# Performance work log

Measured on AMD Instinct MI355X. Metric: run time of the kernel, lower is better.

Reference implementation:

```python
import jax, jax.numpy as jnp
import numpy as np

N = 100000   # nodes
E = 3200000  # edges
IN = 5
H = 128
L = 6
EPS = 1e-5

def _bn(x, g, b):
    # BatchNorm1d in training mode: batch stats over node dim, biased variance
    m = jnp.mean(x, axis=0)
    v = jnp.mean((x - m) ** 2, axis=0)
    return (x - m) * jax.lax.rsqrt(v + EPS) * g + b

def setup_inputs() -> dict:
    key = jax.random.key(0)
    ks = jax.random.split(key, 20)
    x = jax.random.normal(ks[0], (N, IN), dtype=jnp.float32)
    edge_index = jax.random.randint(ks[1], (2, E), 0, N, dtype=jnp.int64)
    batch = jnp.zeros((N,), dtype=jnp.int64)
    s = 0.05
    return {
        "x": x, "edge_index": edge_index, "batch": batch,
        "in_W": jax.random.normal(ks[2], (IN, H), jnp.float32) * s,
        "in_b": jnp.zeros((H,), jnp.float32),
        "in_g": jnp.ones((H,), jnp.float32),
        "in_beta": jnp.zeros((H,), jnp.float32),
        "conv_W": jax.random.normal(ks[3], (L, H, H), jnp.float32) * s,
        "conv_b": jnp.zeros((L, H), jnp.float32),
        "bn_g": jnp.ones((L, H), jnp.float32),
        "bn_beta": jnp.zeros((L, H), jnp.float32),
        "pW1": jax.random.normal(ks[4], (H, 32), jnp.float32) * s,
        "pb1": jnp.zeros((32,), jnp.float32),
        "pW2": jax.random.normal(ks[5], (32, 1), jnp.float32) * s,
        "pb2": jnp.zeros((1,), jnp.float32),
        "vW1": jax.random.normal(ks[6], (H, 64), jnp.float32) * s,
        "vb1": jnp.zeros((64,), jnp.float32),
        "vW2": jax.random.normal(ks[7], (64, 1), jnp.float32) * s,
        "vb2": jnp.zeros((1,), jnp.float32),
    }

def reference(x, edge_index, batch, in_W, in_b, in_g, in_beta,
              conv_W, conv_b, bn_g, bn_beta,
              pW1, pb1, pW2, pb2, vW1, vb1, vW2, vb2):
    n = x.shape[0]
    # GCN normalization with self-loops (computed once; depends only on edge_index)
    loops = jnp.arange(n, dtype=edge_index.dtype)
    src = jnp.concatenate([edge_index[0], loops])
    dst = jnp.concatenate([edge_index[1], loops])
    deg = jax.ops.segment_sum(jnp.ones_like(dst, dtype=x.dtype), dst, num_segments=n)
    dinv = jnp.where(deg > 0, jax.lax.rsqrt(deg), 0.0)
    norm = dinv[src] * dinv[dst]  # [E+N]

    def gcn(h, W, b):
        h = h @ W
        msg = h[src] * norm[:, None]
        return jax.ops.segment_sum(msg, dst, num_segments=n) + b

    h = jax.nn.relu(_bn(x @ in_W + in_b, in_g, in_beta))
    for i in range(L):
        h = jax.nn.relu(_bn(gcn(h, conv_W[i], conv_b[i]), bn_g[i], bn_beta[i])) + h

    policy_logits = (jax.nn.relu(h @ pW1 + pb1) @ pW2 + pb2)[:, 0]  # [N]

    # global_mean_pool over batch ids (single graph here, num_segments=1)
    num_graphs = 1
    sums = jax.ops.segment_sum(h, batch, num_segments=num_graphs)
    cnts = jax.ops.segment_sum(jnp.ones((n,), h.dtype), batch, num_segments=num_graphs)
    g = sums / jnp.maximum(cnts, 1.0)[:, None]  # [1, H]
    value = jnp.tanh(jax.nn.relu(g @ vW1 + vb1) @ vW2 + vb2)[:, 0]  # [1]
    return policy_logits, value
```

## Files before the change

### kernel.cpp

```cpp
#include <hip/hip_runtime.h>
#include <hip/hip_bf16.h>

typedef __hip_bfloat16 bf16;
typedef long long i64;
typedef unsigned short u16;
typedef __attribute__((ext_vector_type(8))) short bf16x8;
typedef __attribute__((ext_vector_type(4))) float f32x4;

#define EPSV 1e-5f
#define WINLEN 2560
#define CHUNK 64

static __device__ __forceinline__ float ldf(const void* p, size_t i, int fb) {
  return fb ? __bfloat162float(((const bf16*)p)[i]) : ((const float*)p)[i];
}
static __device__ __forceinline__ u16 f2b(float f) {
  unsigned int u = __float_as_uint(f);
  u += 0x7FFF + ((u >> 16) & 1);
  return (u16)(u >> 16);
}
static __device__ __forceinline__ float rb2f(u16 u) {
  return __uint_as_float(((unsigned int)u) << 16);
}
static __device__ __forceinline__ unsigned pk2(float a, float b) {
  return (unsigned)f2b(a) | ((unsigned)f2b(b) << 16);
}
static __device__ __forceinline__ float lo2f(unsigned w) { return __uint_as_float(w << 16); }
static __device__ __forceinline__ float hi2f(unsigned w) { return __uint_as_float(w & 0xFFFF0000u); }


__global__ void setup_kernel(const int* __restrict__ ei_w, const unsigned int* __restrict__ g,
                             int* __restrict__ eflag, int* __restrict__ fflag,
                             int* __restrict__ degcnt, int* __restrict__ fill,
                             int* __restrict__ wctr, int n) {
  int i = blockIdx.x * 256 + threadIdx.x;
  if (i < n) { degcnt[i] = 0; fill[i] = 0; }
  if (blockIdx.x == 0) {
    __shared__ int nz;
    if (threadIdx.x == 0) nz = 0;
    if (threadIdx.x < 32) wctr[threadIdx.x] = 0;
    __syncthreads();
    for (int k = threadIdx.x; k < 1024; k += 256)
      if (ei_w[2 * k + 1] != 0) atomicAdd(&nz, 1);
    __syncthreads();
    if (threadIdx.x == 0) {
      *eflag = (nz == 0) ? 1 : 0;
      *fflag = (g[0] == 0x3F803F80u) ? 1 : 0;
    }
  }
}


__global__ void __launch_bounds__(256) pre_merged_kernel(
    const void* __restrict__ x, const void* __restrict__ W, const void* __restrict__ b,
    const void* __restrict__ ei, const void* __restrict__ convW,
    const int* __restrict__ eflag, const int* __restrict__ fflag,
    int* __restrict__ degcnt, u16* __restrict__ pre, float* __restrict__ pi,
    u16* __restrict__ wf, int n, int in_dim, int e, int wtotal, int gi, int gf) {
  __shared__ float4 SS[256], QQ[256];
  int fb = *fflag;
  if ((int)blockIdx.x < gi) {
    int q = threadIdx.x & 31, g8 = threadIdx.x >> 5;
    int c = q * 4;
    float b0 = ldf(b, c, fb), b1 = ldf(b, c + 1, fb), b2v = ldf(b, c + 2, fb), b3 = ldf(b, c + 3, fb);
    float s0 = 0, s1 = 0, s2 = 0, s3 = 0, q0 = 0, q1 = 0, q2 = 0, q3 = 0;
    for (int node = blockIdx.x * 8 + g8; node < n; node += gi * 8) {
      float a0 = b0, a1 = b1, a2 = b2v, a3 = b3;
      for (int k = 0; k < in_dim; ++k) {
        float xv = ldf(x, (size_t)node * in_dim + k, fb);
        size_t w0 = (size_t)k * 128 + c;
        a0 = fmaf(xv, ldf(W, w0, fb), a0);
        a1 = fmaf(xv, ldf(W, w0 + 1, fb), a1);
        a2 = fmaf(xv, ldf(W, w0 + 2, fb), a2);
        a3 = fmaf(xv, ldf(W, w0 + 3, fb), a3);
      }
      unsigned w0p = pk2(a0, a1), w1p = pk2(a2, a3);
      *(uint2*)(pre + (size_t)node * 128 + c) = make_uint2(w0p, w1p);
      float r0 = lo2f(w0p), r1 = hi2f(w0p), r2 = lo2f(w1p), r3 = hi2f(w1p);
      s0 += r0; s1 += r1; s2 += r2; s3 += r3;
      q0 = fmaf(r0, r0, q0); q1 = fmaf(r1, r1, q1); q2 = fmaf(r2, r2, q2); q3 = fmaf(r3, r3, q3);
    }
    SS[threadIdx.x] = make_float4(s0, s1, s2, s3);
    QQ[threadIdx.x] = make_float4(q0, q1, q2, q3);
    __syncthreads();
    if (threadIdx.x < 32) {
      float4 a = SS[threadIdx.x], qq = QQ[threadIdx.x];
      for (int g = 1; g < 8; ++g) {
        float4 u = SS[g * 32 + threadIdx.x], w = QQ[g * 32 + threadIdx.x];
        a.x += u.x; a.y += u.y; a.z += u.z; a.w += u.w;
        qq.x += w.x; qq.y += w.y; qq.z += w.z; qq.w += w.w;
      }
      int cc = threadIdx.x * 4;
      *(float4*)(pi + (size_t)blockIdx.x * 256 + cc) = a;
      *(float4*)(pi + (size_t)blockIdx.x * 256 + 128 + cc) = qq;
    }
  } else if ((int)blockIdx.x < gi + gf) {
    int bid = blockIdx.x - gi;
    int k = bid & 7;
    int lo = (int)(((long long)n * k) >> 3);
    int hi = (int)(((long long)n * (k + 1)) >> 3);
    int stride = (gf >> 3) * 256;
    int fb64 = *eflag;
    for (int i = (bid >> 3) * 256 + threadIdx.x; i < e; i += stride) {
      int d;
      if (fb64) d = (int)((const i64*)ei)[(size_t)e + i];
      else      d = ((const int*)ei)[(size_t)e + i];
      if (d >= lo && d < hi) atomicAdd(&degcnt[d], 1);
    }
  } else {
    int bid = blockIdx.x - gi - gf;
    int i = bid * 256 + threadIdx.x;
    if (i < wtotal) {
      int l = i >> 14, r = i & 16383;
      int k = r >> 7, nn = r & 127;
      int s = k >> 5, quad = (k >> 3) & 3, j = k & 7;
      int ct = nn >> 4, n16 = nn & 15;
      wf[(size_t)l * 16384 + (ct * 4 + s) * 512 + quad * 128 + n16 * 8 + j] = f2b(ldf(convW, i, fb));
    }
  }
}


__global__ void __launch_bounds__(256) scanA_kernel(const int* __restrict__ deg,
                                                    int* __restrict__ rp,
                                                    int* __restrict__ bsum,
                                                    float* __restrict__ dinv, int n) {
  int base = blockIdx.x * 1024 + threadIdx.x * 4;
  int v0 = (base     < n) ? deg[base]     : 0;
  int v1 = (base + 1 < n) ? deg[base + 1] : 0;
  int v2 = (base + 2 < n) ? deg[base + 2] : 0;
  int v3 = (base + 3 < n) ? deg[base + 3] : 0;
  if (base     < n) dinv[base]     = rsqrtf((float)v0 + 1.0f);
  if (base + 1 < n) dinv[base + 1] = rsqrtf((float)v1 + 1.0f);
  if (base + 2 < n) dinv[base + 2] = rsqrtf((float)v2 + 1.0f);
  if (base + 3 < n) dinv[base + 3] = rsqrtf((float)v3 + 1.0f);
  int ts = v0 + v1 + v2 + v3;
  __shared__ int ls[256];
  ls[threadIdx.x] = ts;
  __syncthreads();
  for (int off = 1; off < 256; off <<= 1) {
    int u = (threadIdx.x >= off) ? ls[threadIdx.x - off] : 0;
    __syncthreads();
    ls[threadIdx.x] += u;
    __syncthreads();
  }
  int run = ls[threadIdx.x] - ts;
  if (base     < n) rp[base]     = run; run += v0;
  if (base + 1 < n) rp[base + 1] = run; run += v1;
  if (base + 2 < n) rp[base + 2] = run; run += v2;
  if (base + 3 < n) rp[base + 3] = run;
  if (threadIdx.x == 255) bsum[blockIdx.x] = ls[255];
}

__global__ void __launch_bounds__(256) scanB_kernel(int* __restrict__ bsum, int* __restrict__ rp,
                                                    int nb, int n, int e) {
  __shared__ int ls[256];
  int t = threadIdx.x;
  int v = (t < nb) ? bsum[t] : 0;
  ls[t] = v;
  __syncthreads();
  for (int off = 1; off < 256; off <<= 1) {
    int u = (t >= off) ? ls[t - off] : 0;
    __syncthreads();
    ls[t] += u;
    __syncthreads();
  }
  if (t < nb) bsum[t] = ls[t] - v;
  if (t == 0) rp[n] = e;
}

__global__ void scanC_kernel(int* __restrict__ rp, const int* __restrict__ bsum, int n) {
  int i = blockIdx.x * 256 + threadIdx.x;
  if (i < n) rp[i] += bsum[i >> 10];
}

__global__ void fill_kernel(const void* __restrict__ ei, const int* __restrict__ flag,
                            const int* __restrict__ row_ptr,
                            int* __restrict__ fill, int* __restrict__ csr_src, int e, int n) {
  int k = blockIdx.x & 7;
  int lo = (int)(((long long)n * k) >> 3);
  int hi = (int)(((long long)n * (k + 1)) >> 3);
  int stride = (gridDim.x >> 3) * 256;
  int fb64 = *flag;
  for (int i = (blockIdx.x >> 3) * 256 + threadIdx.x; i < e; i += stride) {
    int d;
    if (fb64) d = (int)((const i64*)ei)[(size_t)e + i];
    else      d = ((const int*)ei)[(size_t)e + i];
    if (d < lo || d >= hi) continue;
    int s;
    if (fb64) s = (int)((const i64*)ei)[i];
    else      s = ((const int*)ei)[i];
    int pos = row_ptr[d] + atomicAdd(&fill[d], 1);
    csr_src[pos] = s;
  }
}

__global__ void __launch_bounds__(1024) finalize_inproj_kernel(
    const float* __restrict__ pi, int nb,
    const void* __restrict__ g, const void* __restrict__ beta,
    const int* __restrict__ fflag,
    float* __restrict__ scale, float* __restrict__ shift,
    float inv_n) {
  __shared__ float RS[8][128], RQ[8][128];
  int fb = *fflag;
  int c = threadIdx.x & 127, r = threadIdx.x >> 7;
  float s = 0.f, s2 = 0.f;
#pragma unroll 4
  for (int b = r; b < nb; b += 8) {
    s  += pi[(size_t)b * 256 + c];
    s2 += pi[(size_t)b * 256 + 128 + c];
  }
  RS[r][c] = s; RQ[r][c] = s2;
  __syncthreads();
  if (threadIdx.x < 128) {
    float ts = 0.f, tq = 0.f;
#pragma unroll
    for (int i = 0; i < 8; ++i) { ts += RS[i][c]; tq += RQ[i][c]; }
    float mean = ts * inv_n;
    float var = tq * inv_n - mean * mean;
    float sc = ldf(g, c, fb) * rsqrtf(var + EPSV);
    scale[c] = sc;
    shift[c] = ldf(beta, c, fb) - mean * sc;
  }
}


__global__ void __launch_bounds__(256) gemm_bn_kernel(
    const u16* __restrict__ pre, u16* __restrict__ hbuf,
    const float* __restrict__ scale, const float* __restrict__ shift,
    const u16* __restrict__ wfL, const float* __restrict__ dinv,
    u16* __restrict__ u, int n, int use_res) {
  __shared__ u16 At[4][2048];
  int lane = threadIdx.x & 63;
  int wave = threadIdx.x >> 6;
  int n16 = lane & 15, quad = lane >> 4;
  u16* at = At[wave];
  int node = lane & 15;
  int cgrp = lane >> 4;
  int ntiles = (n + 15) >> 4;
  for (int tile = blockIdx.x * 4 + wave; tile < ntiles; tile += gridDim.x * 4) {
    int n0 = tile * 16;
    int gn = n0 + node;
#pragma unroll
    for (int r = 0; r < 8; ++r) {
      int c4 = r * 4 + cgrp;
      int c = c4 * 4;
      float4 h4 = make_float4(0.f, 0.f, 0.f, 0.f);
      if (gn < n) {
        uint2 pv = *(const uint2*)(pre + (size_t)gn * 128 + c);
        float4 sc = *(const float4*)(scale + c);
        float4 sh = *(const float4*)(shift + c);
        h4.x = fmaxf(fmaf(lo2f(pv.x), sc.x, sh.x), 0.f);
        h4.y = fmaxf(fmaf(hi2f(pv.x), sc.y, sh.y), 0.f);
        h4.z = fmaxf(fmaf(lo2f(pv.y), sc.z, sh.z), 0.f);
        h4.w = fmaxf(fmaf(hi2f(pv.y), sc.w, sh.w), 0.f);
        if (use_res) {
          uint2 rv = *(const uint2*)(hbuf + (size_t)gn * 128 + c);
          h4.x += lo2f(rv.x); h4.y += hi2f(rv.x);
          h4.z += lo2f(rv.y); h4.w += hi2f(rv.y);
        }
        *(uint2*)(hbuf + (size_t)gn * 128 + c) = make_uint2(pk2(h4.x, h4.y), pk2(h4.z, h4.w));
      }
      ushort4 uu;
      uu.x = f2b(h4.x); uu.y = f2b(h4.y); uu.z = f2b(h4.z); uu.w = f2b(h4.w);
      int s = c4 >> 3, qd = (c4 >> 1) & 3, j0 = (c4 & 1) * 4;
      *(ushort4*)(at + s * 512 + qd * 128 + node * 8 + j0) = uu;
    }
    __builtin_amdgcn_s_waitcnt(0);
    f32x4 acc[8];
#pragma unroll
    for (int ct = 0; ct < 8; ++ct) acc[ct] = (f32x4){0.f, 0.f, 0.f, 0.f};
#pragma unroll
    for (int s = 0; s < 4; ++s) {
      bf16x8 af = *(const bf16x8*)(at + s * 512 + lane * 8);
#pragma unroll
      for (int ct = 0; ct < 8; ++ct) {
        bf16x8 bfr = *(const bf16x8*)(wfL + (size_t)(ct * 4 + s) * 512 + lane * 8);
        acc[ct] = __builtin_amdgcn_mfma_f32_16x16x32_bf16(af, bfr, acc[ct], 0, 0, 0);
      }
    }
    float dv[4];
#pragma unroll
    for (int r = 0; r < 4; ++r) {
      int row = n0 + quad * 4 + r;
      dv[r] = (row < n) ? dinv[row] : 0.f;
    }
#pragma unroll
    for (int ct = 0; ct < 8; ++ct) {
#pragma unroll
      for (int r = 0; r < 4; ++r) {
        int row = n0 + quad * 4 + r;
        if (row < n)
          u[((size_t)(ct >> 1) * n + row) * 32 + (ct & 1) * 16 + n16] = f2b(acc[ct][r] * dv[r]);
      }
    }
  }
}


__global__ void __launch_bounds__(256) gather_stats_kernel(
    const int* __restrict__ row_ptr, const int* __restrict__ csr_src,
    const u16* __restrict__ u, const float* __restrict__ dinv,
    const void* __restrict__ b, const int* __restrict__ fflag,
    u16* __restrict__ pre, float* __restrict__ pg,
    int* __restrict__ wctr, int n, int nch, size_t bOff) {
  __shared__ int sm[WINLEN];
  __shared__ float SW[4][4][8], QW[4][4][8];
  __shared__ int curchunk;
  int fb = *fflag;
  int ct2 = blockIdx.x & 3;
  const u16* us = u + (size_t)ct2 * n * 32;
  int q = threadIdx.x & 3;
  int g = threadIdx.x >> 2;
  int c = ct2 * 32 + q * 8;
  float bias[8];
#pragma unroll
  for (int i = 0; i < 8; ++i) bias[i] = ldf(b, bOff + c + i, fb);
  float sA[8], qA[8];
#pragma unroll
  for (int i = 0; i < 8; ++i) { sA[i] = 0.f; qA[i] = 0.f; }

  for (;;) {
    __syncthreads();
    if (threadIdx.x == 0) curchunk = atomicAdd(&wctr[ct2], 1);
    __syncthreads();
    int ch = curchunk;
    if (ch >= nch) break;
    int c0 = ch * CHUNK;
    int node = c0 + g;
    int valid = node < n;
    int beg = valid ? row_ptr[node] : 0;
    int end = valid ? row_ptr[node + 1] : 0;
    int cend = c0 + CHUNK; if (cend > n) cend = n;
    int chunk_lo = row_ptr[c0];
    int chunk_hi = row_ptr[cend];
    float acc[8];
    if (valid) {
      uint4 su = *(const uint4*)(us + (size_t)node * 32 + q * 8);
      acc[0] = lo2f(su.x); acc[1] = hi2f(su.x);
      acc[2] = lo2f(su.y); acc[3] = hi2f(su.y);
      acc[4] = lo2f(su.z); acc[5] = hi2f(su.z);
      acc[6] = lo2f(su.w); acc[7] = hi2f(su.w);
    } else {
#pragma unroll
      for (int i = 0; i < 8; ++i) acc[i] = 0.f;
    }
    for (int wlo = chunk_lo; wlo < chunk_hi; wlo += WINLEN) {
      int wlen = chunk_hi - wlo; if (wlen > WINLEN) wlen = WINLEN;
      __syncthreads();
      for (int i = threadIdx.x; i < wlen; i += 256)
        sm[i] = __builtin_nontemporal_load(csr_src + wlo + i);
      __syncthreads();
      int j0 = beg > wlo ? beg : wlo;
      int j1 = end < wlo + wlen ? end : wlo + wlen;
      int j = j0;
#define ACC(UU) \
      acc[0] += lo2f(UU.x); acc[1] += hi2f(UU.x); \
      acc[2] += lo2f(UU.y); acc[3] += hi2f(UU.y); \
      acc[4] += lo2f(UU.z); acc[5] += hi2f(UU.z); \
      acc[6] += lo2f(UU.w); acc[7] += hi2f(UU.w);
      for (; j + 8 <= j1; j += 8) {
        int i0 = sm[j - wlo],     i1 = sm[j - wlo + 1], i2 = sm[j - wlo + 2], i3 = sm[j - wlo + 3];
        int i4 = sm[j - wlo + 4], i5 = sm[j - wlo + 5], i6 = sm[j - wlo + 6], i7 = sm[j - wlo + 7];
        uint4 U0 = *(const uint4*)(us + (size_t)i0 * 32 + q * 8);
        uint4 U1 = *(const uint4*)(us + (size_t)i1 * 32 + q * 8);
        uint4 U2 = *(const uint4*)(us + (size_t)i2 * 32 + q * 8);
        uint4 U3 = *(const uint4*)(us + (size_t)i3 * 32 + q * 8);
        uint4 U4 = *(const uint4*)(us + (size_t)i4 * 32 + q * 8);
        uint4 U5 = *(const uint4*)(us + (size_t)i5 * 32 + q * 8);
        uint4 U6 = *(const uint4*)(us + (size_t)i6 * 32 + q * 8);
        uint4 U7 = *(const uint4*)(us + (size_t)i7 * 32 + q * 8);
        ACC(U0) ACC(U1) ACC(U2) ACC(U3) ACC(U4) ACC(U5) ACC(U6) ACC(U7)
      }
      for (; j + 4 <= j1; j += 4) {
        int i0 = sm[j - wlo], i1 = sm[j - wlo + 1], i2 = sm[j - wlo + 2], i3 = sm[j - wlo + 3];
        uint4 U0 = *(const uint4*)(us + (size_t)i0 * 32 + q * 8);
        uint4 U1 = *(const uint4*)(us + (size_t)i1 * 32 + q * 8);
        uint4 U2 = *(const uint4*)(us + (size_t)i2 * 32 + q * 8);
        uint4 U3 = *(const uint4*)(us + (size_t)i3 * 32 + q * 8);
        ACC(U0) ACC(U1) ACC(U2) ACC(U3)
      }
      for (; j < j1; ++j) {
        int i0 = sm[j - wlo];
        uint4 U0 = *(const uint4*)(us + (size_t)i0 * 32 + q * 8);
        ACC(U0)
      }
#undef ACC
    }
    if (valid) {
      float dv = dinv[node];
      float o0 = fmaf(acc[0], dv, bias[0]), o1 = fmaf(acc[1], dv, bias[1]);
      float o2 = fmaf(acc[2], dv, bias[2]), o3 = fmaf(acc[3], dv, bias[3]);
      float o4 = fmaf(acc[4], dv, bias[4]), o5 = fmaf(acc[5], dv, bias[5]);
      float o6 = fmaf(acc[6], dv, bias[6]), o7 = fmaf(acc[7], dv, bias[7]);
      unsigned w0 = pk2(o0, o1), w1 = pk2(o2, o3), w2 = pk2(o4, o5), w3 = pk2(o6, o7);
      *(uint4*)(pre + (size_t)node * 128 + c) = make_uint4(w0, w1, w2, w3);
      float r0 = lo2f(w0), r1 = hi2f(w0), r2 = lo2f(w1), r3 = hi2f(w1);
      float r4 = lo2f(w2), r5 = hi2f(w2), r6 = lo2f(w3), r7 = hi2f(w3);
      sA[0] += r0; sA[1] += r1; sA[2] += r2; sA[3] += r3;
      sA[4] += r4; sA[5] += r5; sA[6] += r6; sA[7] += r7;
      qA[0] = fmaf(r0, r0, qA[0]); qA[1] = fmaf(r1, r1, qA[1]);
      qA[2] = fmaf(r2, r2, qA[2]); qA[3] = fmaf(r3, r3, qA[3]);
      qA[4] = fmaf(r4, r4, qA[4]); qA[5] = fmaf(r5, r5, qA[5]);
      qA[6] = fmaf(r6, r6, qA[6]); qA[7] = fmaf(r7, r7, qA[7]);
    }
  }
#pragma unroll
  for (int m = 4; m <= 32; m <<= 1) {
#pragma unroll
    for (int i = 0; i < 8; ++i) {
      sA[i] += __shfl_xor(sA[i], m, 64);
      qA[i] += __shfl_xor(qA[i], m, 64);
    }
  }
  int lane = threadIdx.x & 63, wv = threadIdx.x >> 6;
  if (lane < 4) {
#pragma unroll
    for (int i = 0; i < 8; ++i) { SW[wv][lane][i] = sA[i]; QW[wv][lane][i] = qA[i]; }
  }
  __syncthreads();
  if (threadIdx.x < 32) {
    int qq = threadIdx.x >> 3, i = threadIdx.x & 7;
    float a = SW[0][qq][i] + SW[1][qq][i] + SW[2][qq][i] + SW[3][qq][i];
    float b2 = QW[0][qq][i] + QW[1][qq][i] + QW[2][qq][i] + QW[3][qq][i];
    pg[(size_t)blockIdx.x * 64 + qq * 8 + i] = a;
    pg[(size_t)blockIdx.x * 64 + 32 + qq * 8 + i] = b2;
  }
}

__global__ void __launch_bounds__(1024) finalize_gather_kernel(
    const float* __restrict__ pg, int nbG,
    const void* __restrict__ g, const void* __restrict__ beta,
    const int* __restrict__ fflag,
    float* __restrict__ scale, float* __restrict__ shift,
    float inv_n, size_t off) {
  __shared__ float RS[8][128], RQ[8][128];
  int fb = *fflag;
  int c = threadIdx.x & 127, r = threadIdx.x >> 7;
  int ct2 = c >> 5, ic = c & 31;
  float s = 0.f, s2 = 0.f;
#pragma unroll 4
  for (int b = ct2 + 4 * r; b < nbG; b += 32) {
    s  += pg[(size_t)b * 64 + ic];
    s2 += pg[(size_t)b * 64 + 32 + ic];
  }
  RS[r][c] = s; RQ[r][c] = s2;
  __syncthreads();
  if (threadIdx.x < 128) {
    float ts = 0.f, tq = 0.f;
#pragma unroll
    for (int i = 0; i < 8; ++i) { ts += RS[i][c]; tq += RQ[i][c]; }
    float mean = ts * inv_n;
    float var = tq * inv_n - mean * mean;
    float sc = ldf(g, off + c, fb) * rsqrtf(var + EPSV);
    scale[c] = sc;
    shift[c] = ldf(beta, off + c, fb) - mean * sc;
  }
}


__global__ void __launch_bounds__(256) policy_pool_kernel(
    const u16* __restrict__ pre, const u16* __restrict__ hbuf,
    const float* __restrict__ scale, const float* __restrict__ shift,
    const void* __restrict__ pW1, const void* __restrict__ pb1,
    const void* __restrict__ pW2, const void* __restrict__ pb2,
    const int* __restrict__ fflag, float* __restrict__ pp,
    void* __restrict__ out, int n) {
  __shared__ float W1[128 * 32];
  __shared__ float B1v[32], W2v[32];
  int fb = *fflag;
  for (int i = threadIdx.x; i < 128 * 32; i += 256) W1[i] = ldf(pW1, i, fb);
  if (threadIdx.x < 32) {
    B1v[threadIdx.x] = ldf(pb1, threadIdx.x, fb);
    W2v[threadIdx.x] = ldf(pW2, threadIdx.x, fb);
  }
  __syncthreads();
  float bias2 = ldf(pb2, 0, fb);
  int q = threadIdx.x & 31, g8 = threadIdx.x >> 5;
  int c = q * 4;
  float4 sc = *(const float4*)(scale + c);
  float4 sh = *(const float4*)(shift + c);
  float cs0 = 0, cs1 = 0, cs2 = 0, cs3 = 0;
  for (int node = blockIdx.x * 8 + g8; node < n; node += gridDim.x * 8) {
    uint2 pv = *(const uint2*)(pre + (size_t)node * 128 + c);
    uint2 rv = *(const uint2*)(hbuf + (size_t)node * 128 + c);
    float4 h4;
    h4.x = fmaxf(fmaf(lo2f(pv.x), sc.x, sh.x), 0.f) + lo2f(rv.x);
    h4.y = fmaxf(fmaf(hi2f(pv.x), sc.y, sh.y), 0.f) + hi2f(rv.x);
    h4.z = fmaxf(fmaf(lo2f(pv.y), sc.z, sh.z), 0.f) + lo2f(rv.y);
    h4.w = fmaxf(fmaf(hi2f(pv.y), sc.w, sh.w), 0.f) + hi2f(rv.y);
    cs0 += h4.x; cs1 += h4.y; cs2 += h4.z; cs3 += h4.w;
    float acc = B1v[q];
#pragma unroll
    for (int k4 = 0; k4 < 32; ++k4) {
      float hx = __shfl(h4.x, k4, 32);
      float hy = __shfl(h4.y, k4, 32);
      float hz = __shfl(h4.z, k4, 32);
      float hw = __shfl(h4.w, k4, 32);
      int k = k4 * 4;
      acc = fmaf(hx, W1[k * 32 + q], acc);
      acc = fmaf(hy, W1[(k + 1) * 32 + q], acc);
      acc = fmaf(hz, W1[(k + 2) * 32 + q], acc);
      acc = fmaf(hw, W1[(k + 3) * 32 + q], acc);
    }
    acc = fmaxf(acc, 0.f) * W2v[q];
    for (int off = 16; off; off >>= 1) acc += __shfl_down(acc, off, 32);
    if (q == 0) {
      float v = acc + bias2;
      if (fb) ((bf16*)out)[node] = __float2bfloat16(v);
      else    ((float*)out)[node] = v;
    }
  }
  __shared__ float4 SS[256];
  SS[threadIdx.x] = make_float4(cs0, cs1, cs2, cs3);
  __syncthreads();
  if (threadIdx.x < 32) {
    float4 a = SS[threadIdx.x];
    for (int g = 1; g < 8; ++g) {
      float4 u = SS[g * 32 + threadIdx.x];
      a.x += u.x; a.y += u.y; a.z += u.z; a.w += u.w;
    }
    *(float4*)(pp + (size_t)blockIdx.x * 128 + threadIdx.x * 4) = a;
  }
}

__global__ void __launch_bounds__(1024) value_kernel(
    const float* __restrict__ pp, int nbP,
    const void* __restrict__ vW1, const void* __restrict__ vb1,
    const void* __restrict__ vW2, const void* __restrict__ vb2,
    const int* __restrict__ fflag,
    void* __restrict__ out, int n, float inv_n) {
  __shared__ float RS[8][128];
  __shared__ float gs[128];
  int fb = *fflag;
  int c = threadIdx.x & 127, r = threadIdx.x >> 7;
  float s = 0.f;
#pragma unroll 4
  for (int b = r; b < nbP; b += 8) s += pp[(size_t)b * 128 + c];
  RS[r][c] = s;
  __syncthreads();
  if (threadIdx.x < 128) {
    float t = 0.f;
#pragma unroll
    for (int i = 0; i < 8; ++i) t += RS[i][c];
    gs[c] = t;
  }
  __syncthreads();
  if (threadIdx.x < 64) {
    int cc = threadIdx.x;
    float acc = ldf(vb1, cc, fb);
    for (int k = 0; k < 128; ++k) acc = fmaf(gs[k] * inv_n, ldf(vW1, (size_t)k * 64 + cc, fb), acc);
    acc = fmaxf(acc, 0.f);
    float v = acc * ldf(vW2, cc, fb);
    for (int off = 32; off; off >>= 1) v += __shfl_down(v, off, 64);
    if (cc == 0) {
      float rr = tanhf(v + ldf(vb2, 0, fb));
      if (fb) ((bf16*)out)[n] = __float2bfloat16(rr);
      else    ((float*)out)[n] = rr;
    }
  }
}


extern "C" void kernel_launch(void* const* d_in, const int* in_sizes, int n_in,
                              void* d_out, int out_size, void* d_ws, size_t ws_size,
                              hipStream_t stream) {
  const void* x       = d_in[0];
  const void* ei      = d_in[1];
  const void* in_W    = d_in[3];
  const void* in_b    = d_in[4];
  const void* in_g    = d_in[5];
  const void* in_beta = d_in[6];
  const void* conv_W  = d_in[7];
  const void* conv_b  = d_in[8];
  const void* bn_g    = d_in[9];
  const void* bn_beta = d_in[10];
  const void* pW1     = d_in[11];
  const void* pb1     = d_in[12];
  const void* pW2     = d_in[13];
  const void* pb2     = d_in[14];
  const void* vW1     = d_in[15];
  const void* vb1     = d_in[16];
  const void* vW2     = d_in[17];
  const void* vb2     = d_in[18];

  const int H = 128;
  int in_dim = in_sizes[3] / H;
  int n      = in_sizes[0] / in_dim;
  int e      = in_sizes[1] / 2;
  int L      = in_sizes[7] / (H * H);

  const int GS  = 2048;
  const int GI  = 512;
  const int GP  = 1024;
  const int GF  = 2048;

  char* w = (char*)d_ws;
  u16*   u    = (u16*)w;   w += (size_t)n * H * sizeof(u16);
  u16*   pre  = (u16*)w;   w += (size_t)n * H * sizeof(u16);
  u16*   hbuf = (u16*)w;   w += (size_t)n * H * sizeof(u16);
  int*   csr_src  = (int*)w;   w += ((size_t)e + 16) * sizeof(int);
  int*   row_ptr  = (int*)w;   w += (size_t)(n + 1 + 15) / 16 * 16 * sizeof(int);
  int*   degcnt   = (int*)w;   w += (size_t)n * sizeof(int);
  int*   fillc    = (int*)w;   w += (size_t)n * sizeof(int);
  float* dinv     = (float*)w; w += (size_t)n * sizeof(float);
  float* scale = (float*)w; w += 128 * sizeof(float);
  float* shift = (float*)w; w += 128 * sizeof(float);
  int*   eflag = (int*)w;   w += 16 * sizeof(int);
  int*   fflag = (int*)w;   w += 16 * sizeof(int);
  int*   bsum  = (int*)w;   w += 256 * sizeof(int);
  int*   wctr  = (int*)w;   w += 32 * sizeof(int);
  u16*   wf    = (u16*)w;   w += (size_t)L * H * H * sizeof(u16);
  float* pi    = (float*)w; w += (size_t)GI * 256 * sizeof(float);
  float* pg    = (float*)w; w += (size_t)GS * 64 * sizeof(float);
  float* pp    = (float*)w; w += (size_t)GP * 128 * sizeof(float);

  int gN = (n + 255) / 256;
  int nb = (n + 1023) >> 10;
  int nch = (n + CHUNK - 1) / CHUNK;
  int wtotal = L * H * H;
  int GW = (wtotal + 255) / 256;
  float inv_n = 1.0f / (float)n;

  setup_kernel<<<gN, 256, 0, stream>>>((const int*)ei, (const unsigned int*)in_g,
                                       eflag, fflag, degcnt, fillc, wctr, n);
  pre_merged_kernel<<<GI + GF + GW, 256, 0, stream>>>(
      x, in_W, in_b, ei, conv_W, eflag, fflag, degcnt, pre, pi, wf,
      n, in_dim, e, wtotal, GI, GF);
  scanA_kernel<<<nb, 256, 0, stream>>>(degcnt, row_ptr, bsum, dinv, n);
  scanB_kernel<<<1, 256, 0, stream>>>(bsum, row_ptr, nb, n, e);
  scanC_kernel<<<gN, 256, 0, stream>>>(row_ptr, bsum, n);
  fill_kernel<<<GF, 256, 0, stream>>>(ei, eflag, row_ptr, fillc, csr_src, e, n);
  finalize_inproj_kernel<<<1, 1024, 0, stream>>>(pi, GI, in_g, in_beta, fflag, scale, shift, inv_n);

  for (int l = 0; l < L; ++l) {
    gemm_bn_kernel<<<2048, 256, 0, stream>>>(pre, hbuf, scale, shift, wf + (size_t)l * H * H,
                                             dinv, u, n, (l > 0) ? 1 : 0);
    gather_stats_kernel<<<GS, 256, 0, stream>>>(row_ptr, csr_src, u, dinv,
                                                conv_b, fflag, pre, pg, wctr + l * 4,
                                                n, nch, (size_t)l * H);
    finalize_gather_kernel<<<1, 1024, 0, stream>>>(pg, GS, bn_g, bn_beta, fflag, scale, shift,
                                                   inv_n, (size_t)l * H);
  }

  policy_pool_kernel<<<GP, 256, 0, stream>>>(pre, hbuf, scale, shift, pW1, pb1, pW2, pb2,
                                             fflag, pp, d_out, n);
  value_kernel<<<1, 1024, 0, stream>>>(pp, GP, vW1, vb1, vW2, vb2, fflag, d_out, n, inv_n);
}
```

Before: 1.721 ms.

## Fold BN finalize and value kernels into neighbors via atomic stat accumulation

Result: faster. 1.685 ms (-2.1%).

```diff
diff --git a/kernel.cpp b/kernel.cpp
--- a/kernel.cpp
+++ b/kernel.cpp
@@ -6,6 +6,7 @@
 typedef unsigned short u16;
 typedef __attribute__((ext_vector_type(8))) short bf16x8;
 typedef __attribute__((ext_vector_type(4))) float f32x4;
+typedef __attribute__((ext_vector_type(2))) long long ll2;
 
 #define EPSV 1e-5f
 #define WINLEN 2560
@@ -19,9 +20,6 @@
   u += 0x7FFF + ((u >> 16) & 1);
   return (u16)(u >> 16);
 }
-static __device__ __forceinline__ float rb2f(u16 u) {
-  return __uint_as_float(((unsigned int)u) << 16);
-}
 static __device__ __forceinline__ unsigned pk2(float a, float b) {
   return (unsigned)f2b(a) | ((unsigned)f2b(b) << 16);
 }
@@ -32,13 +30,17 @@
 __global__ void setup_kernel(const int* __restrict__ ei_w, const unsigned int* __restrict__ g,
                              int* __restrict__ eflag, int* __restrict__ fflag,
                              int* __restrict__ degcnt, int* __restrict__ fill,
-                             int* __restrict__ wctr, int n) {
+                             int* __restrict__ wctr, int* __restrict__ pctr,
+                             float* __restrict__ buf0, float* __restrict__ buf1,
+                             float* __restrict__ ppacc, int n) {
   int i = blockIdx.x * 256 + threadIdx.x;
   if (i < n) { degcnt[i] = 0; fill[i] = 0; }
   if (blockIdx.x == 0) {
     __shared__ int nz;
-    if (threadIdx.x == 0) nz = 0;
+    if (threadIdx.x == 0) { nz = 0; *pctr = 0; }
     if (threadIdx.x < 32) wctr[threadIdx.x] = 0;
+    buf0[threadIdx.x] = 0.f; buf1[threadIdx.x] = 0.f;
+    if (threadIdx.x < 128) ppacc[threadIdx.x] = 0.f;
     __syncthreads();
     for (int k = threadIdx.x; k < 1024; k += 256)
       if (ei_w[2 * k + 1] != 0) atomicAdd(&nz, 1);
@@ -55,7 +57,7 @@
     const void* __restrict__ x, const void* __restrict__ W, const void* __restrict__ b,
     const void* __restrict__ ei, const void* __restrict__ convW,
     const int* __restrict__ eflag, const int* __restrict__ fflag,
-    int* __restrict__ degcnt, u16* __restrict__ pre, float* __restrict__ pi,
+    int* __restrict__ degcnt, u16* __restrict__ pre, float* __restrict__ acc0,
     u16* __restrict__ wf, int n, int in_dim, int e, int wtotal, int gi, int gf) {
   __shared__ float4 SS[256], QQ[256];
   int fb = *fflag;
@@ -85,27 +87,48 @@
     __syncthreads();
     if (threadIdx.x < 32) {
       float4 a = SS[threadIdx.x], qq = QQ[threadIdx.x];
-      for (int g = 1; g < 8; ++g) {
-        float4 u = SS[g * 32 + threadIdx.x], w = QQ[g * 32 + threadIdx.x];
+      for (int g2 = 1; g2 < 8; ++g2) {
+        float4 u = SS[g2 * 32 + threadIdx.x], w = QQ[g2 * 32 + threadIdx.x];
         a.x += u.x; a.y += u.y; a.z += u.z; a.w += u.w;
         qq.x += w.x; qq.y += w.y; qq.z += w.z; qq.w += w.w;
       }
       int cc = threadIdx.x * 4;
-      *(float4*)(pi + (size_t)blockIdx.x * 256 + cc) = a;
-      *(float4*)(pi + (size_t)blockIdx.x * 256 + 128 + cc) = qq;
+      atomicAdd(&acc0[cc + 0], a.x); atomicAdd(&acc0[cc + 1], a.y);
+      atomicAdd(&acc0[cc + 2], a.z); atomicAdd(&acc0[cc + 3], a.w);
+      atomicAdd(&acc0[128 + cc + 0], qq.x); atomicAdd(&acc0[128 + cc + 1], qq.y);
+      atomicAdd(&acc0[128 + cc + 2], qq.z); atomicAdd(&acc0[128 + cc + 3], qq.w);
     }
   } else if ((int)blockIdx.x < gi + gf) {
     int bid = blockIdx.x - gi;
     int k = bid & 7;
     int lo = (int)(((long long)n * k) >> 3);
     int hi = (int)(((long long)n * (k + 1)) >> 3);
-    int stride = (gf >> 3) * 256;
+    int stride = (gf >> 3) * 1024;
     int fb64 = *eflag;
-    for (int i = (bid >> 3) * 256 + threadIdx.x; i < e; i += stride) {
-      int d;
-      if (fb64) d = (int)((const i64*)ei)[(size_t)e + i];
-      else      d = ((const int*)ei)[(size_t)e + i];
-      if (d >= lo && d < hi) atomicAdd(&degcnt[d], 1);
+    for (int i = (bid >> 3) * 1024 + threadIdx.x * 4; i < e; i += stride) {
+      int d0, d1, d2, d3; int cnt;
+      if (i + 3 < e) {
+        cnt = 4;
+        if (fb64) {
+          ll2 a = *(const ll2*)((const i64*)ei + (size_t)e + i);
+          ll2 b2 = *(const ll2*)((const i64*)ei + (size_t)e + i + 2);
+          d0 = (int)a.x; d1 = (int)a.y; d2 = (int)b2.x; d3 = (int)b2.y;
+        } else {
+          int4 dv = *(const int4*)((const int*)ei + (size_t)e + i);
+          d0 = dv.x; d1 = dv.y; d2 = dv.z; d3 = dv.w;
+        }
+      } else {
+        cnt = e - i; d0 = d1 = d2 = d3 = -1;
+        for (int j = 0; j < cnt; ++j) {
+          int dj = fb64 ? (int)((const i64*)ei)[(size_t)e + i + j]
+                        : ((const int*)ei)[(size_t)e + i + j];
+          if (j == 0) d0 = dj; else if (j == 1) d1 = dj; else if (j == 2) d2 = dj; else d3 = dj;
+        }
+      }
+      if (d0 >= lo && d0 < hi) atomicAdd(&degcnt[d0], 1);
+      if (d1 >= lo && d1 < hi) atomicAdd(&degcnt[d1], 1);
+      if (d2 >= lo && d2 < hi) atomicAdd(&degcnt[d2], 1);
+      if (d3 >= lo && d3 < hi) atomicAdd(&degcnt[d3], 1);
     }
   } else {
     int bid = blockIdx.x - gi - gf;
@@ -180,57 +203,70 @@
   int k = blockIdx.x & 7;
   int lo = (int)(((long long)n * k) >> 3);
   int hi = (int)(((long long)n * (k + 1)) >> 3);
-  int stride = (gridDim.x >> 3) * 256;
+  int stride = (gridDim.x >> 3) * 1024;
   int fb64 = *flag;
-  for (int i = (blockIdx.x >> 3) * 256 + threadIdx.x; i < e; i += stride) {
-    int d;
-    if (fb64) d = (int)((const i64*)ei)[(size_t)e + i];
-    else      d = ((const int*)ei)[(size_t)e + i];
-    if (d < lo || d >= hi) continue;
-    int s;
-    if (fb64) s = (int)((const i64*)ei)[i];
-    else      s = ((const int*)ei)[i];
-    int pos = row_ptr[d] + atomicAdd(&fill[d], 1);
-    csr_src[pos] = s;
-  }
-}
-
-__global__ void __launch_bounds__(1024) finalize_inproj_kernel(
-    const float* __restrict__ pi, int nb,
-    const void* __restrict__ g, const void* __restrict__ beta,
-    const int* __restrict__ fflag,
-    float* __restrict__ scale, float* __restrict__ shift,
-    float inv_n) {
-  __shared__ float RS[8][128], RQ[8][128];
-  int fb = *fflag;
-  int c = threadIdx.x & 127, r = threadIdx.x >> 7;
-  float s = 0.f, s2 = 0.f;
-#pragma unroll 4
-  for (int b = r; b < nb; b += 8) {
-    s  += pi[(size_t)b * 256 + c];
-    s2 += pi[(size_t)b * 256 + 128 + c];
-  }
-  RS[r][c] = s; RQ[r][c] = s2;
-  __syncthreads();
-  if (threadIdx.x < 128) {
-    float ts = 0.f, tq = 0.f;
-#pragma unroll
-    for (int i = 0; i < 8; ++i) { ts += RS[i][c]; tq += RQ[i][c]; }
-    float mean = ts * inv_n;
-    float var = tq * inv_n - mean * mean;
-    float sc = ldf(g, c, fb) * rsqrtf(var + EPSV);
-    scale[c] = sc;
-    shift[c] = ldf(beta, c, fb) - mean * sc;
+  for (int i = (blockIdx.x >> 3) * 1024 + threadIdx.x * 4; i < e; i += stride) {
+    if (i + 3 < e) {
+      int d0, d1, d2, d3;
+      if (fb64) {
+        ll2 a = *(const ll2*)((const i64*)ei + (size_t)e + i);
+        ll2 b2 = *(const ll2*)((const i64*)ei + (size_t)e + i + 2);
+        d0 = (int)a.x; d1 = (int)a.y; d2 = (int)b2.x; d3 = (int)b2.y;
+      } else {
+        int4 dv = *(const int4*)((const int*)ei + (size_t)e + i);
+        d0 = dv.x; d1 = dv.y; d2 = dv.z; d3 = dv.w;
+      }
+      int in0 = (d0 >= lo && d0 < hi), in1 = (d1 >= lo && d1 < hi);
+      int in2 = (d2 >= lo && d2 < hi), in3 = (d3 >= lo && d3 < hi);
+      if (in0 | in1 | in2 | in3) {
+        int s0, s1, s2, s3;
+        if (fb64) {
+          ll2 sa = *(const ll2*)((const i64*)ei + i);
+          ll2 sb = *(const ll2*)((const i64*)ei + i + 2);
+          s0 = (int)sa.x; s1 = (int)sa.y; s2 = (int)sb.x; s3 = (int)sb.y;
+        } else {
+          int4 sv = *(const int4*)((const int*)ei + i);
+          s0 = sv.x; s1 = sv.y; s2 = sv.z; s3 = sv.w;
+        }
+        if (in0) { int pos = row_ptr[d0] + atomicAdd(&fill[d0], 1); csr_src[pos] = s0; }
+        if (in1) { int pos = row_ptr[d1] + atomicAdd(&fill[d1], 1); csr_src[pos] = s1; }
+        if (in2) { int pos = row_ptr[d2] + atomicAdd(&fill[d2], 1); csr_src[pos] = s2; }
+        if (in3) { int pos = row_ptr[d3] + atomicAdd(&fill[d3], 1); csr_src[pos] = s3; }
+      }
+    } else {
+      for (int j = 0; i + j < e; ++j) {
+        int d = fb64 ? (int)((const i64*)ei)[(size_t)e + i + j] : ((const int*)ei)[(size_t)e + i + j];
+        if (d < lo || d >= hi) continue;
+        int s = fb64 ? (int)((const i64*)ei)[i + j] : ((const int*)ei)[i + j];
+        int pos = row_ptr[d] + atomicAdd(&fill[d], 1);
+        csr_src[pos] = s;
+      }
+    }
   }
 }
 
 
 __global__ void __launch_bounds__(256) gemm_bn_kernel(
     const u16* __restrict__ pre, u16* __restrict__ hbuf,
-    const float* __restrict__ scale, const float* __restrict__ shift,
+    const float* __restrict__ accIn, float* __restrict__ accZ,
+    const void* __restrict__ g, const void* __restrict__ beta, const int* __restrict__ fflag,
     const u16* __restrict__ wfL, const float* __restrict__ dinv,
-    u16* __restrict__ u, int n, int use_res) {
+    u16* __restrict__ u, int n, int use_res, float inv_n, int gOff) {
   __shared__ u16 At[4][2048];
+  __shared__ float SC[128], SH[128];
+  int fb = *fflag;
+  if (threadIdx.x < 128) {
+    int c = threadIdx.x;
+    float s = accIn[c], s2 = accIn[128 + c];
+    float mean = s * inv_n;
+    float var = s2 * inv_n - mean * mean;
+    float sc = ldf(g, (size_t)gOff + c, fb) * rsqrtf(var + EPSV);
+    SC[c] = sc;
+    SH[c] = ldf(beta, (size_t)gOff + c, fb) - mean * sc;
+  }
+  if (blockIdx.x == 0) accZ[threadIdx.x] = 0.f;
+  __syncthreads();
+
   int lane = threadIdx.x & 63;
   int wave = threadIdx.x >> 6;
   int n16 = lane & 15, quad = lane >> 4;
@@ -242,29 +278,34 @@
     int n0 = tile * 16;
     int gn = n0 + node;
 #pragma unroll
-    for (int r = 0; r < 8; ++r) {
-      int c4 = r * 4 + cgrp;
-      int c = c4 * 4;
-      float4 h4 = make_float4(0.f, 0.f, 0.f, 0.f);
+    for (int r = 0; r < 4; ++r) {
+      int c8 = r * 4 + cgrp;
+      int c = c8 * 8;
+      uint4 ww = make_uint4(0u, 0u, 0u, 0u);
       if (gn < n) {
-        uint2 pv = *(const uint2*)(pre + (size_t)gn * 128 + c);
-        float4 sc = *(const float4*)(scale + c);
-        float4 sh = *(const float4*)(shift + c);
-        h4.x = fmaxf(fmaf(lo2f(pv.x), sc.x, sh.x), 0.f);
-        h4.y = fmaxf(fmaf(hi2f(pv.x), sc.y, sh.y), 0.f);
-        h4.z = fmaxf(fmaf(lo2f(pv.y), sc.z, sh.z), 0.f);
-        h4.w = fmaxf(fmaf(hi2f(pv.y), sc.w, sh.w), 0.f);
+        uint4 pv = *(const uint4*)(pre + (size_t)gn * 128 + c);
+        unsigned pw[4] = {pv.x, pv.y, pv.z, pv.w};
+        float h[8];
+#pragma unroll
+        for (int m = 0; m < 4; ++m) {
+          h[2 * m]     = fmaxf(fmaf(lo2f(pw[m]), SC[c + 2 * m],     SH[c + 2 * m]), 0.f);
+          h[2 * m + 1] = fmaxf(fmaf(hi2f(pw[m]), SC[c + 2 * m + 1], SH[c + 2 * m + 1]), 0.f);
+        }
         if (use_res) {
-          uint2 rv = *(const uint2*)(hbuf + (size_t)gn * 128 + c);
-          h4.x += lo2f(rv.x); h4.y += hi2f(rv.x);
-          h4.z += lo2f(rv.y); h4.w += hi2f(rv.y);
+          uint4 rv = *(const uint4*)(hbuf + (size_t)gn * 128 + c);
+          unsigned rw[4] = {rv.x, rv.y, rv.z, rv.w};
+#pragma unroll
+          for (int m = 0; m < 4; ++m) {
+            h[2 * m] += lo2f(rw[m]); h[2 * m + 1] += hi2f(rw[m]);
+          }
         }
-        *(uint2*)(hbuf + (size_t)gn * 128 + c) = make_uint2(pk2(h4.x, h4.y), pk2(h4.z, h4.w));
-      }
-      ushort4 uu;
-      uu.x = f2b(h4.x); uu.y = f2b(h4.y); uu.z = f2b(h4.z); uu.w = f2b(h4.w);
-      int s = c4 >> 3, qd = (c4 >> 1) & 3, j0 = (c4 & 1) * 4;
-      *(ushort4*)(at + s * 512 + qd * 128 + node * 8 + j0) = uu;
+        ww.x = pk2(h[0], h[1]); ww.y = pk2(h[2], h[3]);
+        ww.z = pk2(h[4], h[5]); ww.w = pk2(h[6], h[7]);
+        *(uint4*)(hbuf + (size_t)gn * 128 + c) = ww;
+      }
+      int c4 = c8 * 2;
+      int s = c4 >> 3, qd = (c4 >> 1) & 3;
+      *(uint4*)(at + s * 512 + qd * 128 + node * 8) = ww;
     }
     __builtin_amdgcn_s_waitcnt(0);
     f32x4 acc[8];
@@ -302,7 +343,7 @@
     const int* __restrict__ row_ptr, const int* __restrict__ csr_src,
     const u16* __restrict__ u, const float* __restrict__ dinv,
     const void* __restrict__ b, const int* __restrict__ fflag,
-    u16* __restrict__ pre, float* __restrict__ pg,
+    u16* __restrict__ pre, float* __restrict__ accOut,
     int* __restrict__ wctr, int n, int nch, size_t bOff) {
   __shared__ int sm[WINLEN];
   __shared__ float SW[4][4][8], QW[4][4][8];
@@ -423,63 +464,48 @@
     int qq = threadIdx.x >> 3, i = threadIdx.x & 7;
     float a = SW[0][qq][i] + SW[1][qq][i] + SW[2][qq][i] + SW[3][qq][i];
     float b2 = QW[0][qq][i] + QW[1][qq][i] + QW[2][qq][i] + QW[3][qq][i];
-    pg[(size_t)blockIdx.x * 64 + qq * 8 + i] = a;
-    pg[(size_t)blockIdx.x * 64 + 32 + qq * 8 + i] = b2;
-  }
-}
-
-__global__ void __launch_bounds__(1024) finalize_gather_kernel(
-    const float* __restrict__ pg, int nbG,
-    const void* __restrict__ g, const void* __restrict__ beta,
-    const int* __restrict__ fflag,
-    float* __restrict__ scale, float* __restrict__ shift,
-    float inv_n, size_t off) {
-  __shared__ float RS[8][128], RQ[8][128];
-  int fb = *fflag;
-  int c = threadIdx.x & 127, r = threadIdx.x >> 7;
-  int ct2 = c >> 5, ic = c & 31;
-  float s = 0.f, s2 = 0.f;
-#pragma unroll 4
-  for (int b = ct2 + 4 * r; b < nbG; b += 32) {
-    s  += pg[(size_t)b * 64 + ic];
-    s2 += pg[(size_t)b * 64 + 32 + ic];
-  }
-  RS[r][c] = s; RQ[r][c] = s2;
-  __syncthreads();
-  if (threadIdx.x < 128) {
-    float ts = 0.f, tq = 0.f;
-#pragma unroll
-    for (int i = 0; i < 8; ++i) { ts += RS[i][c]; tq += RQ[i][c]; }
-    float mean = ts * inv_n;
-    float var = tq * inv_n - mean * mean;
-    float sc = ldf(g, off + c, fb) * rsqrtf(var + EPSV);
-    scale[c] = sc;
-    shift[c] = ldf(beta, off + c, fb) - mean * sc;
+    int chn = ct2 * 32 + qq * 8 + i;
+    atomicAdd(&accOut[chn], a);
+    atomicAdd(&accOut[128 + chn], b2);
   }
 }
 
 
 __global__ void __launch_bounds__(256) policy_pool_kernel(
     const u16* __restrict__ pre, const u16* __restrict__ hbuf,
-    const float* __restrict__ scale, const float* __restrict__ shift,
+    const float* __restrict__ accIn,
+    const void* __restrict__ bg, const void* __restrict__ bbeta, int gOff,
     const void* __restrict__ pW1, const void* __restrict__ pb1,
     const void* __restrict__ pW2, const void* __restrict__ pb2,
-    const int* __restrict__ fflag, float* __restrict__ pp,
-    void* __restrict__ out, int n) {
+    const void* __restrict__ vW1, const void* __restrict__ vb1,
+    const void* __restrict__ vW2, const void* __restrict__ vb2,
+    const int* __restrict__ fflag, float* __restrict__ ppacc, int* __restrict__ pctr,
+    void* __restrict__ out, int n, float inv_n) {
   __shared__ float W1[128 * 32];
   __shared__ float B1v[32], W2v[32];
+  __shared__ float SC[128], SH[128];
+  __shared__ int plast;
   int fb = *fflag;
   for (int i = threadIdx.x; i < 128 * 32; i += 256) W1[i] = ldf(pW1, i, fb);
   if (threadIdx.x < 32) {
     B1v[threadIdx.x] = ldf(pb1, threadIdx.x, fb);
     W2v[threadIdx.x] = ldf(pW2, threadIdx.x, fb);
   }
+  if (threadIdx.x < 128) {
+    int cch = threadIdx.x;
+    float s = accIn[cch], s2 = accIn[128 + cch];
+    float mean = s * inv_n;
+    float var = s2 * inv_n - mean * mean;
+    float sc = ldf(bg, (size_t)gOff + cch, fb) * rsqrtf(var + EPSV);
+    SC[cch] = sc;
+    SH[cch] = ldf(bbeta, (size_t)gOff + cch, fb) - mean * sc;
+  }
   __syncthreads();
   float bias2 = ldf(pb2, 0, fb);
   int q = threadIdx.x & 31, g8 = threadIdx.x >> 5;
   int c = q * 4;
-  float4 sc = *(const float4*)(scale + c);
-  float4 sh = *(const float4*)(shift + c);
+  float4 sc = *(const float4*)&SC[c];
+  float4 sh = *(const float4*)&SH[c];
   float cs0 = 0, cs1 = 0, cs2 = 0, cs3 = 0;
   for (int node = blockIdx.x * 8 + g8; node < n; node += gridDim.x * 8) {
     uint2 pv = *(const uint2*)(pre + (size_t)node * 128 + c);
@@ -516,47 +542,37 @@
   __syncthreads();
   if (threadIdx.x < 32) {
     float4 a = SS[threadIdx.x];
-    for (int g = 1; g < 8; ++g) {
-      float4 u = SS[g * 32 + threadIdx.x];
+    for (int g2 = 1; g2 < 8; ++g2) {
+      float4 u = SS[g2 * 32 + threadIdx.x];
       a.x += u.x; a.y += u.y; a.z += u.z; a.w += u.w;
     }
-    *(float4*)(pp + (size_t)blockIdx.x * 128 + threadIdx.x * 4) = a;
-  }
-}
-
-__global__ void __launch_bounds__(1024) value_kernel(
-    const float* __restrict__ pp, int nbP,
-    const void* __restrict__ vW1, const void* __restrict__ vb1,
-    const void* __restrict__ vW2, const void* __restrict__ vb2,
-    const int* __restrict__ fflag,
-    void* __restrict__ out, int n, float inv_n) {
-  __shared__ float RS[8][128];
-  __shared__ float gs[128];
-  int fb = *fflag;
-  int c = threadIdx.x & 127, r = threadIdx.x >> 7;
-  float s = 0.f;
-#pragma unroll 4
-  for (int b = r; b < nbP; b += 8) s += pp[(size_t)b * 128 + c];
-  RS[r][c] = s;
-  __syncthreads();
-  if (threadIdx.x < 128) {
-    float t = 0.f;
-#pragma unroll
-    for (int i = 0; i < 8; ++i) t += RS[i][c];
-    gs[c] = t;
-  }
-  __syncthreads();
-  if (threadIdx.x < 64) {
-    int cc = threadIdx.x;
-    float acc = ldf(vb1, cc, fb);
-    for (int k = 0; k < 128; ++k) acc = fmaf(gs[k] * inv_n, ldf(vW1, (size_t)k * 64 + cc, fb), acc);
-    acc = fmaxf(acc, 0.f);
-    float v = acc * ldf(vW2, cc, fb);
-    for (int off = 32; off; off >>= 1) v += __shfl_down(v, off, 64);
-    if (cc == 0) {
-      float rr = tanhf(v + ldf(vb2, 0, fb));
-      if (fb) ((bf16*)out)[n] = __float2bfloat16(rr);
-      else    ((float*)out)[n] = rr;
+    int cc = threadIdx.x * 4;
+    atomicAdd(&ppacc[cc + 0], a.x); atomicAdd(&ppacc[cc + 1], a.y);
+    atomicAdd(&ppacc[cc + 2], a.z); atomicAdd(&ppacc[cc + 3], a.w);
+  }
+  __syncthreads();
+  if (threadIdx.x == 0) {
+    int old = atomicAdd(pctr, 1);
+    plast = (old == (int)gridDim.x - 1) ? 1 : 0;
+  }
+  __syncthreads();
+  if (plast) {
+    __shared__ float gs[128];
+    if (threadIdx.x < 128) gs[threadIdx.x] = atomicAdd(&ppacc[threadIdx.x], 0.f);
+    __syncthreads();
+    if (threadIdx.x < 64) {
+      int cc = threadIdx.x;
+      float acc2 = ldf(vb1, cc, fb);
+      for (int k = 0; k < 128; ++k)
+        acc2 = fmaf(gs[k] * inv_n, ldf(vW1, (size_t)k * 64 + cc, fb), acc2);
+      acc2 = fmaxf(acc2, 0.f);
+      float v = acc2 * ldf(vW2, cc, fb);
+      for (int off = 32; off; off >>= 1) v += __shfl_down(v, off, 64);
+      if (cc == 0) {
+        float rr = tanhf(v + ldf(vb2, 0, fb));
+        if (fb) ((bf16*)out)[n] = __float2bfloat16(rr);
+        else    ((float*)out)[n] = rr;
+      }
     }
   }
 }
@@ -604,16 +620,15 @@
   int*   degcnt   = (int*)w;   w += (size_t)n * sizeof(int);
   int*   fillc    = (int*)w;   w += (size_t)n * sizeof(int);
   float* dinv     = (float*)w; w += (size_t)n * sizeof(float);
-  float* scale = (float*)w; w += 128 * sizeof(float);
-  float* shift = (float*)w; w += 128 * sizeof(float);
   int*   eflag = (int*)w;   w += 16 * sizeof(int);
   int*   fflag = (int*)w;   w += 16 * sizeof(int);
   int*   bsum  = (int*)w;   w += 256 * sizeof(int);
   int*   wctr  = (int*)w;   w += 32 * sizeof(int);
+  int*   pctr  = (int*)w;   w += 16 * sizeof(int);
+  float* buf0  = (float*)w; w += 256 * sizeof(float);
+  float* buf1  = (float*)w; w += 256 * sizeof(float);
+  float* ppacc = (float*)w; w += 128 * sizeof(float);
   u16*   wf    = (u16*)w;   w += (size_t)L * H * H * sizeof(u16);
-  float* pi    = (float*)w; w += (size_t)GI * 256 * sizeof(float);
-  float* pg    = (float*)w; w += (size_t)GS * 64 * sizeof(float);
-  float* pp    = (float*)w; w += (size_t)GP * 128 * sizeof(float);
 
   int gN = (n + 255) / 256;
   int nb = (n + 1023) >> 10;
@@ -621,29 +636,33 @@
   int wtotal = L * H * H;
   int GW = (wtotal + 255) / 256;
   float inv_n = 1.0f / (float)n;
+  float* bufs[2] = {buf0, buf1};
 
   setup_kernel<<<gN, 256, 0, stream>>>((const int*)ei, (const unsigned int*)in_g,
-                                       eflag, fflag, degcnt, fillc, wctr, n);
+                                       eflag, fflag, degcnt, fillc, wctr, pctr,
+                                       buf0, buf1, ppacc, n);
   pre_merged_kernel<<<GI + GF + GW, 256, 0, stream>>>(
-      x, in_W, in_b, ei, conv_W, eflag, fflag, degcnt, pre, pi, wf,
+      x, in_W, in_b, ei, conv_W, eflag, fflag, degcnt, pre, buf0, wf,
       n, in_dim, e, wtotal, GI, GF);
   scanA_kernel<<<nb, 256, 0, stream>>>(degcnt, row_ptr, bsum, dinv, n);
   scanB_kernel<<<1, 256, 0, stream>>>(bsum, row_ptr, nb, n, e);
   scanC_kernel<<<gN, 256, 0, stream>>>(row_ptr, bsum, n);
   fill_kernel<<<GF, 256, 0, stream>>>(ei, eflag, row_ptr, fillc, csr_src, e, n);
-  finalize_inproj_kernel<<<1, 1024, 0, stream>>>(pi, GI, in_g, in_beta, fflag, scale, shift, inv_n);
 
   for (int l = 0; l < L; ++l) {
-    gemm_bn_kernel<<<2048, 256, 0, stream>>>(pre, hbuf, scale, shift, wf + (size_t)l * H * H,
-                                             dinv, u, n, (l > 0) ? 1 : 0);
+    const void* g    = (l == 0) ? in_g    : bn_g;
+    const void* beta = (l == 0) ? in_beta : bn_beta;
+    int gOff = (l == 0) ? 0 : (l - 1) * H;
+    gemm_bn_kernel<<<2048, 256, 0, stream>>>(pre, hbuf, bufs[l & 1], bufs[(l + 1) & 1],
+                                             g, beta, fflag, wf + (size_t)l * H * H,
+                                             dinv, u, n, (l > 0) ? 1 : 0, inv_n, gOff);
     gather_stats_kernel<<<GS, 256, 0, stream>>>(row_ptr, csr_src, u, dinv,
-                                                conv_b, fflag, pre, pg, wctr + l * 4,
-                                                n, nch, (size_t)l * H);
-    finalize_gather_kernel<<<1, 1024, 0, stream>>>(pg, GS, bn_g, bn_beta, fflag, scale, shift,
-                                                   inv_n, (size_t)l * H);
-  }
-
-  policy_pool_kernel<<<GP, 256, 0, stream>>>(pre, hbuf, scale, shift, pW1, pb1, pW2, pb2,
-                                             fflag, pp, d_out, n);
-  value_kernel<<<1, 1024, 0, stream>>>(pp, GP, vW1, vb1, vW2, vb2, fflag, d_out, n, inv_n);
-}
+                                                conv_b, fflag, pre, bufs[(l + 1) & 1],
+                                                wctr + l * 4, n, nch, (size_t)l * H);
+  }
+
+  policy_pool_kernel<<<GP, 256, 0, stream>>>(pre, hbuf, bufs[L & 1],
+                                             bn_g, bn_beta, (L - 1) * H,
+                                             pW1, pb1, pW2, pb2, vW1, vb1, vW2, vb2,
+                                             fflag, ppacc, pctr, d_out, n, inv_n);
+}
```
